# Kernel tuning notes

Measured on AMD Instinct MI355X. Metric: run time of the kernel, lower is better.

The kernel has to match this reference:

```python
import jax, jax.numpy as jnp
import numpy as np

SQ, B, NP, HN = 2048, 2, 16, 64  # [seq, batch, heads, head_dim]

def setup_inputs() -> dict:
    key = jax.random.key(0)
    kq, kk, kv = jax.random.split(key, 3)
    return {
        "query": jax.random.normal(kq, (SQ, B, NP, HN), dtype=jnp.float32),
        "key":   jax.random.normal(kk, (SQ, B, NP, HN), dtype=jnp.float32),
        "value": jax.random.normal(kv, (SQ, B, NP, HN), dtype=jnp.float32),
    }

def reference(query, key, value):
    sq, b, nheads, hn = query.shape
    # NOTE: original module computes norm_factor=sqrt(hn) but never applies it;
    # scores are UNscaled QK^T, replicated faithfully here.
    scores = jnp.einsum('sbnh,tbnh->bnst', query, key)          # [b, np, sq, sk]
    probs = jax.nn.softmax(scores, axis=-1)                      # mask=None -> plain softmax
    # dropout is deterministic (train=False default) -> identity
    context = jnp.einsum('bnst,tbnh->sbnh', probs, value)        # [sq, b, np, hn]
    return context.reshape(sq, b, nheads * hn).astype(jnp.float32)
```

## Files before the change

### kernel.cpp

```cpp
#include <hip/hip_runtime.h>
#include <math.h>
#include <stdint.h>

#define SQ 2048
#define NBH 32
#define HN 64
#define BQ 128
#define BK2 128
#define NP2 (SQ/BK2)
#define TOK 2048
#define HSTRIDE (SQ*HN)

typedef _Float16 half2v __attribute__((ext_vector_type(2)));
typedef _Float16 half4v __attribute__((ext_vector_type(4)));
typedef _Float16 half8v __attribute__((ext_vector_type(8)));
typedef float f32x16 __attribute__((ext_vector_type(16)));

__device__ __forceinline__ void async16(const void* g, void* l) {
  __builtin_amdgcn_global_load_lds(
      (const __attribute__((address_space(1))) void*)g,
      (__attribute__((address_space(3))) void*)l, 16, 0, 0);
}

__device__ __forceinline__ float fexp2(float x) {
#if __has_builtin(__builtin_amdgcn_exp2f)
  return __builtin_amdgcn_exp2f(x);
#else
  return exp2f(x);
#endif
}

__device__ __forceinline__ float xmax32(float x) {
#if __has_builtin(__builtin_amdgcn_permlane32_swap)
  auto r = __builtin_amdgcn_permlane32_swap(__float_as_int(x), __float_as_int(x),
                                            false, false);
  return fmaxf(__int_as_float(r[0]), __int_as_float(r[1]));
#else
  return fmaxf(x, __shfl_xor(x, 32, 64));
#endif
}
__device__ __forceinline__ float xadd32(float x) {
#if __has_builtin(__builtin_amdgcn_permlane32_swap)
  auto r = __builtin_amdgcn_permlane32_swap(__float_as_int(x), __float_as_int(x),
                                            false, false);
  return __int_as_float(r[0]) + __int_as_float(r[1]);
#else
  return x + __shfl_xor(x, 32, 64);
#endif
}

__global__ __launch_bounds__(256) void prep_kv(const float* __restrict__ K,
                                               const float* __restrict__ V,
                                               _Float16* __restrict__ Kh,
                                               _Float16* __restrict__ Vt) {
  __shared__ _Float16 vs[HN * 64];
  const int t = threadIdx.x;
  const int head = blockIdx.y;
  {
    const int key = blockIdx.x * 64 + (t >> 2);
    const int c0 = (t & 3) * 2;
    const float* src = K + (size_t)key * TOK + head * HN + c0 * 8;
    float4 a = *(const float4*)src;
    float4 b = *(const float4*)(src + 4);
    float4 c = *(const float4*)(src + 8);
    float4 d = *(const float4*)(src + 12);
    half8v h0, h1;
    h0[0]=(_Float16)a.x; h0[1]=(_Float16)a.y; h0[2]=(_Float16)a.z; h0[3]=(_Float16)a.w;
    h0[4]=(_Float16)b.x; h0[5]=(_Float16)b.y; h0[6]=(_Float16)b.z; h0[7]=(_Float16)b.w;
    h1[0]=(_Float16)c.x; h1[1]=(_Float16)c.y; h1[2]=(_Float16)c.z; h1[3]=(_Float16)c.w;
    h1[4]=(_Float16)d.x; h1[5]=(_Float16)d.y; h1[6]=(_Float16)d.z; h1[7]=(_Float16)d.w;
    _Float16* row = Kh + (size_t)head * HSTRIDE + (size_t)key * 64;
    *(half8v*)&row[((c0    ) ^ (key & 7)) * 8] = h0;
    *(half8v*)&row[((c0 + 1) ^ (key & 7)) * 8] = h1;
  }
  {
    const int kt = blockIdx.x * 64;
    const int kl = (t >> 3) * 2;
    const int db = (t & 7) * 8;
    const float* src = V + (size_t)(kt + kl) * TOK + head * HN + db;
    float4 a0 = *(const float4*)src;
    float4 a1 = *(const float4*)(src + 4);
    float4 b0 = *(const float4*)(src + TOK);
    float4 b1 = *(const float4*)(src + TOK + 4);
    const float av[8] = {a0.x,a0.y,a0.z,a0.w,a1.x,a1.y,a1.z,a1.w};
    const float bv[8] = {b0.x,b0.y,b0.z,b0.w,b1.x,b1.y,b1.z,b1.w};
    const int u = kl >> 2;
    #pragma unroll
    for (int j = 0; j < 8; ++j) {
      const int dim = db + j;
      const int pos = u ^ (dim & 15);
      half2v h; h[0] = (_Float16)av[j]; h[1] = (_Float16)bv[j];
      *(half2v*)&vs[dim * 64 + pos * 4 + (kl & 3)] = h;
    }
    __syncthreads();
    const int dim = t >> 2;
    const int q = (t & 3) ^ (dim & 3);
    const _Float16* srow = &vs[dim * 64 + q * 16];
    _Float16* drow = Vt + (size_t)head * HSTRIDE + (size_t)dim * SQ + kt + q * 16;
    *(half8v*)&drow[0] = *(const half8v*)&srow[0];
    *(half8v*)&drow[8] = *(const half8v*)&srow[8];
  }
}

__global__ __launch_bounds__(512, 4)
void fattn_mfma(const float* __restrict__ Q, const _Float16* __restrict__ Kh,
                const _Float16* __restrict__ Vt, float* __restrict__ O) {
  __shared__ __align__(16) _Float16 smem[4 * 8192];
  _Float16* kbf = smem;
  _Float16* vtf = smem + 16384;

  const int t = threadIdx.x;
  const int lane = t & 63;
  const int w = t >> 6;
  const int qw = w & 3;
  const int g = w >> 2;
  const int h2 = lane >> 5;
  const int l31 = lane & 31;
  const int q0 = blockIdx.x * BQ + qw * 32;
  const int head = blockIdx.y;
  const _Float16* Kp = Kh + (size_t)head * HSTRIDE;
  const _Float16* Vp = Vt + (size_t)head * HSTRIDE;
  const int tb = g * 4096;

  half8v qf[4];
  {
    const float* qp = Q + (size_t)(q0 + l31) * TOK + head * HN + 8 * h2;
    const float s = 1.44269504088896f;
    #pragma unroll
    for (int ks = 0; ks < 4; ++ks) {
      float4 a = *(const float4*)(qp + 16 * ks);
      float4 b = *(const float4*)(qp + 16 * ks + 4);
      half8v f;
      f[0] = (_Float16)(s*a.x); f[1] = (_Float16)(s*a.y); f[2] = (_Float16)(s*a.z); f[3] = (_Float16)(s*a.w);
      f[4] = (_Float16)(s*b.x); f[5] = (_Float16)(s*b.y); f[6] = (_Float16)(s*b.z); f[7] = (_Float16)(s*b.w);
      qf[ks] = f;
    }
  }

  f32x16 acc0, acc1;
  #pragma unroll
  for (int r = 0; r < 16; ++r) { acc0[r] = 0.f; acc1[r] = 0.f; }
  float m_i = -INFINITY, l_i = 0.f;

  auto stage = [&](int p) {
    const int buf = p & 1;
    const size_t kt = (size_t)p * BK2;
    #pragma unroll
    for (int i = 0; i < 2; ++i) {
      const int off = w * 512 + i * 4096;
      async16(Kp + kt * 64 + off + lane * 8, kbf + buf * 8192 + off);
    }
    #pragma unroll
    for (int tl = 0; tl < 2; ++tl) {
      const int off = w * 512;
      const int eo = off + lane * 8;
      const int dim = eo >> 6, inner = eo & 63;
      async16(Vp + (size_t)dim * SQ + kt + tl * 64 + inner,
              vtf + buf * 8192 + tl * 4096 + off);
    }
  };

  stage(0);
  for (int p = 0; p < NP2; ++p) {
    __syncthreads();
    if (p + 1 < NP2) stage(p + 1);
    const int cur = p & 1;
    const _Float16* kb = kbf + cur * 8192 + tb;
    const _Float16* vb = vtf + cur * 8192 + tb;

    f32x16 c0, c1;
    #pragma unroll
    for (int r = 0; r < 16; ++r) { c0[r] = 0.f; c1[r] = 0.f; }
    #pragma unroll
    for (int ks = 0; ks < 4; ++ks) {
      const int pos = ((h2 + 2 * ks) ^ (l31 & 7)) * 8;
      half8v a0v = *(const half8v*)&kb[l31 * 64 + pos];
      half8v a1v = *(const half8v*)&kb[(l31 + 32) * 64 + pos];
      c0 = __builtin_amdgcn_mfma_f32_32x32x16_f16(a0v, qf[ks], c0, 0, 0, 0);
      c1 = __builtin_amdgcn_mfma_f32_32x32x16_f16(a1v, qf[ks], c1, 0, 0, 0);
    }

    float mx0 = fmaxf(c0[0], c1[0]);
    float mx1 = fmaxf(c0[1], c1[1]);
    float mx2 = fmaxf(c0[2], c1[2]);
    float mx3 = fmaxf(c0[3], c1[3]);
    #pragma unroll
    for (int r = 4; r < 16; r += 4) {
      mx0 = fmaxf(mx0, fmaxf(c0[r],     c1[r]));
      mx1 = fmaxf(mx1, fmaxf(c0[r + 1], c1[r + 1]));
      mx2 = fmaxf(mx2, fmaxf(c0[r + 2], c1[r + 2]));
      mx3 = fmaxf(mx3, fmaxf(c0[r + 3], c1[r + 3]));
    }
    float mx = fmaxf(fmaxf(mx0, mx1), fmaxf(mx2, mx3));
    mx = xmax32(mx);
    const float mnew = fmaxf(m_i, mx);
    const float alpha = fexp2(m_i - mnew);
    float rs0 = 0.f, rs1 = 0.f;
    #pragma unroll
    for (int r = 0; r < 16; ++r) {
      float p0 = fexp2(c0[r] - mnew);
      float p1 = fexp2(c1[r] - mnew);
      c0[r] = p0; c1[r] = p1;
      rs0 += p0; rs1 += p1;
    }
    float rsum = xadd32(rs0 + rs1);
    l_i = l_i * alpha + rsum;
    m_i = mnew;
    #pragma unroll
    for (int r = 0; r < 16; ++r) { acc0[r] *= alpha; acc1[r] *= alpha; }

    #pragma unroll
    for (int ks = 0; ks < 4; ++ks) {
      const int rb = 8 * (ks & 1);
      const f32x16& s = (ks < 2) ? c0 : c1;
      union { half8v v8; half2v v2[4]; } pu;
      #pragma unroll
      for (int tt = 0; tt < 4; ++tt) {
        auto pk = __builtin_amdgcn_cvt_pkrtz(s[rb + 2 * tt], s[rb + 2 * tt + 1]);
        pu.v2[tt] = *(half2v*)&pk;
      }
      #pragma unroll
      for (int mbd = 0; mbd < 2; ++mbd) {
        const int dim = l31 + 32 * mbd;
        const int sw = dim & 15;
        union { half8v v8; half4v v4[2]; } au;
        au.v4[0] = *(const half4v*)&vb[dim * 64 + ((4 * ks + h2)     ^ sw) * 4];
        au.v4[1] = *(const half4v*)&vb[dim * 64 + ((4 * ks + 2 + h2) ^ sw) * 4];
        if (mbd == 0)
          acc0 = __builtin_amdgcn_mfma_f32_32x32x16_f16(au.v8, pu.v8, acc0, 0, 0, 0);
        else
          acc1 = __builtin_amdgcn_mfma_f32_32x32x16_f16(au.v8, pu.v8, acc1, 0, 0, 0);
      }
    }
  }

  __syncthreads();
  float* fb = (float*)smem;
  const int slot = qw * 64 + lane;
  if (g == 1) {
    #pragma unroll
    for (int r = 0; r < 16; ++r) {
      fb[slot * 32 + r]      = acc0[r];
      fb[slot * 32 + 16 + r] = acc1[r];
    }
    fb[8192 + slot] = m_i;
    fb[8448 + slot] = l_i;
  }
  __syncthreads();
  if (g == 0) {
    const float m2 = fb[8192 + slot];
    const float l2 = fb[8448 + slot];
    const float ms = fmaxf(m_i, m2);
    const float a0 = fexp2(m_i - ms);
    const float a1 = fexp2(m2 - ms);
    const float invl = 1.f / (l_i * a0 + l2 * a1);
    float* orow = O + (size_t)(q0 + l31) * TOK + head * HN;
    #pragma unroll
    for (int r = 0; r < 16; ++r) {
      const int d = (r & 3) + 8 * (r >> 2) + 4 * h2;
      orow[d]      = (acc0[r] * a0 + fb[slot * 32 + r]      * a1) * invl;
      orow[d + 32] = (acc1[r] * a0 + fb[slot * 32 + 16 + r] * a1) * invl;
    }
  }
}

extern "C" void kernel_launch(void* const* d_in, const int* in_sizes, int n_in,
                              void* d_out, int out_size, void* d_ws, size_t ws_size,
                              hipStream_t stream) {
  const float* Q = (const float*)d_in[0];
  const float* K = (const float*)d_in[1];
  const float* V = (const float*)d_in[2];
  float* O = (float*)d_out;
  _Float16* Kh = (_Float16*)d_ws;
  _Float16* Vh = Kh + (size_t)NBH * HSTRIDE;
  prep_kv<<<dim3(SQ / 64, NBH), 256, 0, stream>>>(K, V, Kh, Vh);
  fattn_mfma<<<dim3(SQ / BQ, NBH), 512, 0, stream>>>(Q, Kh, Vh, O);
}
```

Measured before the change: 143.0 us.

## Fuse K/V fp16 conversion into attention kernel with register-staged prefetch

Removes the separate prep_kv kernel and its fp16 workspace round trip. The attention kernel now loads fp32 K and V tiles into registers one stage ahead, converts them, and writes them into swizzled/transposed LDS after the softmax step, replacing async global-to-LDS copies. This saves a kernel launch and the extra global traffic. In exchange, each of the 16 query blocks per head rereads fp32 K/V at twice the bytes, register pressure rises (launch bounds drop to 2 blocks), and LDS writes for the V transpose move into the hot loop.

```diff
diff --git a/kernel.cpp b/kernel.cpp
--- a/kernel.cpp
+++ b/kernel.cpp
@@ -9,18 +9,11 @@
 #define BK2 128
 #define NP2 (SQ/BK2)
 #define TOK 2048
-#define HSTRIDE (SQ*HN)
 
 typedef _Float16 half2v __attribute__((ext_vector_type(2)));
 typedef _Float16 half4v __attribute__((ext_vector_type(4)));
 typedef _Float16 half8v __attribute__((ext_vector_type(8)));
 typedef float f32x16 __attribute__((ext_vector_type(16)));
-
-__device__ __forceinline__ void async16(const void* g, void* l) {
-  __builtin_amdgcn_global_load_lds(
-      (const __attribute__((address_space(1))) void*)g,
-      (__attribute__((address_space(3))) void*)l, 16, 0, 0);
-}
 
 __device__ __forceinline__ float fexp2(float x) {
 #if __has_builtin(__builtin_amdgcn_exp2f)
@@ -49,62 +42,9 @@
 #endif
 }
 
-__global__ __launch_bounds__(256) void prep_kv(const float* __restrict__ K,
-                                               const float* __restrict__ V,
-                                               _Float16* __restrict__ Kh,
-                                               _Float16* __restrict__ Vt) {
-  __shared__ _Float16 vs[HN * 64];
-  const int t = threadIdx.x;
-  const int head = blockIdx.y;
-  {
-    const int key = blockIdx.x * 64 + (t >> 2);
-    const int c0 = (t & 3) * 2;
-    const float* src = K + (size_t)key * TOK + head * HN + c0 * 8;
-    float4 a = *(const float4*)src;
-    float4 b = *(const float4*)(src + 4);
-    float4 c = *(const float4*)(src + 8);
-    float4 d = *(const float4*)(src + 12);
-    half8v h0, h1;
-    h0[0]=(_Float16)a.x; h0[1]=(_Float16)a.y; h0[2]=(_Float16)a.z; h0[3]=(_Float16)a.w;
-    h0[4]=(_Float16)b.x; h0[5]=(_Float16)b.y; h0[6]=(_Float16)b.z; h0[7]=(_Float16)b.w;
-    h1[0]=(_Float16)c.x; h1[1]=(_Float16)c.y; h1[2]=(_Float16)c.z; h1[3]=(_Float16)c.w;
-    h1[4]=(_Float16)d.x; h1[5]=(_Float16)d.y; h1[6]=(_Float16)d.z; h1[7]=(_Float16)d.w;
-    _Float16* row = Kh + (size_t)head * HSTRIDE + (size_t)key * 64;
-    *(half8v*)&row[((c0    ) ^ (key & 7)) * 8] = h0;
-    *(half8v*)&row[((c0 + 1) ^ (key & 7)) * 8] = h1;
-  }
-  {
-    const int kt = blockIdx.x * 64;
-    const int kl = (t >> 3) * 2;
-    const int db = (t & 7) * 8;
-    const float* src = V + (size_t)(kt + kl) * TOK + head * HN + db;
-    float4 a0 = *(const float4*)src;
-    float4 a1 = *(const float4*)(src + 4);
-    float4 b0 = *(const float4*)(src + TOK);
-    float4 b1 = *(const float4*)(src + TOK + 4);
-    const float av[8] = {a0.x,a0.y,a0.z,a0.w,a1.x,a1.y,a1.z,a1.w};
-    const float bv[8] = {b0.x,b0.y,b0.z,b0.w,b1.x,b1.y,b1.z,b1.w};
-    const int u = kl >> 2;
-    #pragma unroll
-    for (int j = 0; j < 8; ++j) {
-      const int dim = db + j;
-      const int pos = u ^ (dim & 15);
-      half2v h; h[0] = (_Float16)av[j]; h[1] = (_Float16)bv[j];
-      *(half2v*)&vs[dim * 64 + pos * 4 + (kl & 3)] = h;
-    }
-    __syncthreads();
-    const int dim = t >> 2;
-    const int q = (t & 3) ^ (dim & 3);
-    const _Float16* srow = &vs[dim * 64 + q * 16];
-    _Float16* drow = Vt + (size_t)head * HSTRIDE + (size_t)dim * SQ + kt + q * 16;
-    *(half8v*)&drow[0] = *(const half8v*)&srow[0];
-    *(half8v*)&drow[8] = *(const half8v*)&srow[8];
-  }
-}
-
-__global__ __launch_bounds__(512, 4)
-void fattn_mfma(const float* __restrict__ Q, const _Float16* __restrict__ Kh,
-                const _Float16* __restrict__ Vt, float* __restrict__ O) {
+__global__ __launch_bounds__(512, 2)
+void fattn_fused(const float* __restrict__ Q, const float* __restrict__ K,
+                 const float* __restrict__ V, float* __restrict__ O) {
   __shared__ __align__(16) _Float16 smem[4 * 8192];
   _Float16* kbf = smem;
   _Float16* vtf = smem + 16384;
@@ -118,9 +58,20 @@
   const int l31 = lane & 31;
   const int q0 = blockIdx.x * BQ + qw * 32;
   const int head = blockIdx.y;
-  const _Float16* Kp = Kh + (size_t)head * HSTRIDE;
-  const _Float16* Vp = Vt + (size_t)head * HSTRIDE;
   const int tb = g * 4096;
+
+  const int sk_key = t >> 2;
+  const int sk_c0 = (t & 3) * 2;
+  const int sk_sw0 = ((sk_c0    ) ^ (sk_key & 7)) * 8;
+  const int sk_sw1 = ((sk_c0 + 1) ^ (sk_key & 7)) * 8;
+  const float* ksrc = K + (size_t)sk_key * TOK + head * HN + sk_c0 * 8;
+  const int sv_tl = t >> 8;
+  const int sv_tloc = t & 255;
+  const int sv_kl = (sv_tloc >> 3) * 2;
+  const int sv_db = (sv_tloc & 7) * 8;
+  const int sv_u = sv_kl >> 2;
+  const int sv_k3 = sv_kl & 3;
+  const float* vsrc = V + (size_t)(sv_tl * 64 + sv_kl) * TOK + head * HN + sv_db;
 
   half8v qf[4];
   {
@@ -142,28 +93,52 @@
   for (int r = 0; r < 16; ++r) { acc0[r] = 0.f; acc1[r] = 0.f; }
   float m_i = -INFINITY, l_i = 0.f;
 
-  auto stage = [&](int p) {
+  float4 kr0, kr1, kr2, kr3, vr0, vr1, vr2, vr3;
+
+  auto stage_load = [&](int p) {
+    const size_t off = (size_t)p * BK2 * TOK;
+    const float* ks = ksrc + off;
+    kr0 = *(const float4*)(ks);
+    kr1 = *(const float4*)(ks + 4);
+    kr2 = *(const float4*)(ks + 8);
+    kr3 = *(const float4*)(ks + 12);
+    const float* vs = vsrc + off;
+    vr0 = *(const float4*)(vs);
+    vr1 = *(const float4*)(vs + 4);
+    vr2 = *(const float4*)(vs + TOK);
+    vr3 = *(const float4*)(vs + TOK + 4);
+  };
+  auto stage_write = [&](int p) {
     const int buf = p & 1;
-    const size_t kt = (size_t)p * BK2;
-    #pragma unroll
-    for (int i = 0; i < 2; ++i) {
-      const int off = w * 512 + i * 4096;
-      async16(Kp + kt * 64 + off + lane * 8, kbf + buf * 8192 + off);
-    }
-    #pragma unroll
-    for (int tl = 0; tl < 2; ++tl) {
-      const int off = w * 512;
-      const int eo = off + lane * 8;
-      const int dim = eo >> 6, inner = eo & 63;
-      async16(Vp + (size_t)dim * SQ + kt + tl * 64 + inner,
-              vtf + buf * 8192 + tl * 4096 + off);
+    {
+      half8v h0, h1;
+      h0[0]=(_Float16)kr0.x; h0[1]=(_Float16)kr0.y; h0[2]=(_Float16)kr0.z; h0[3]=(_Float16)kr0.w;
+      h0[4]=(_Float16)kr1.x; h0[5]=(_Float16)kr1.y; h0[6]=(_Float16)kr1.z; h0[7]=(_Float16)kr1.w;
+      h1[0]=(_Float16)kr2.x; h1[1]=(_Float16)kr2.y; h1[2]=(_Float16)kr2.z; h1[3]=(_Float16)kr2.w;
+      h1[4]=(_Float16)kr3.x; h1[5]=(_Float16)kr3.y; h1[6]=(_Float16)kr3.z; h1[7]=(_Float16)kr3.w;
+      _Float16* row = kbf + buf * 8192 + sk_key * 64;
+      *(half8v*)&row[sk_sw0] = h0;
+      *(half8v*)&row[sk_sw1] = h1;
+    }
+    {
+      const float av[8] = {vr0.x,vr0.y,vr0.z,vr0.w,vr1.x,vr1.y,vr1.z,vr1.w};
+      const float bv[8] = {vr2.x,vr2.y,vr2.z,vr2.w,vr3.x,vr3.y,vr3.z,vr3.w};
+      _Float16* vrow = vtf + buf * 8192 + sv_tl * 4096;
+      #pragma unroll
+      for (int j = 0; j < 8; ++j) {
+        const int dim = sv_db + j;
+        const int pos = sv_u ^ (dim & 15);
+        half2v h; h[0] = (_Float16)av[j]; h[1] = (_Float16)bv[j];
+        *(half2v*)&vrow[dim * 64 + pos * 4 + sv_k3] = h;
+      }
     }
   };
 
-  stage(0);
+  stage_load(0);
+  stage_write(0);
   for (int p = 0; p < NP2; ++p) {
     __syncthreads();
-    if (p + 1 < NP2) stage(p + 1);
+    if (p + 1 < NP2) stage_load(p + 1);
     const int cur = p & 1;
     const _Float16* kb = kbf + cur * 8192 + tb;
     const _Float16* vb = vtf + cur * 8192 + tb;
@@ -208,6 +183,8 @@
     m_i = mnew;
     #pragma unroll
     for (int r = 0; r < 16; ++r) { acc0[r] *= alpha; acc1[r] *= alpha; }
+
+    if (p + 1 < NP2) stage_write(p + 1);
 
     #pragma unroll
     for (int ks = 0; ks < 4; ++ks) {
@@ -271,8 +248,6 @@
   const float* K = (const float*)d_in[1];
   const float* V = (const float*)d_in[2];
   float* O = (float*)d_out;
-  _Float16* Kh = (_Float16*)d_ws;
-  _Float16* Vh = Kh + (size_t)NBH * HSTRIDE;
-  prep_kv<<<dim3(SQ / 64, NBH), 256, 0, stream>>>(K, V, Kh, Vh);
-  fattn_mfma<<<dim3(SQ / BQ, NBH), 512, 0, stream>>>(Q, Kh, Vh, O);
-}
+  (void)d_ws; (void)ws_size;
+  fattn_fused<<<dim3(SQ / BQ, NBH), 512, 0, stream>>>(Q, K, V, O);
+}
```

After: 167.3 us. +17.0%, slower.

## Process two 32-row query tiles per wave to reuse K/V LDS fragments

Applied to the files above, without the earlier changes.

Each wave now handles 64 query rows (two 32-row sub-tiles A and B) instead of 32, doubling the block query tile to 256. Each K and V fragment read from LDS feeds two MFMAs, halving LDS traffic and K/V global staging per query row. The cost is doubled accumulator and score register pressure, so launch bounds drop to 2 blocks per CU. The grid also halves to 256 blocks, which may under-fill the GPU, and the epilogue merge becomes serialized with extra barriers.

```diff
diff --git a/kernel.cpp b/kernel.cpp
--- a/kernel.cpp
+++ b/kernel.cpp
@@ -5,7 +5,7 @@
 #define SQ 2048
 #define NBH 32
 #define HN 64
-#define BQ 128
+#define BQ 256
 #define BK2 128
 #define NP2 (SQ/BK2)
 #define TOK 2048
@@ -102,7 +102,7 @@
   }
 }
 
-__global__ __launch_bounds__(512, 4)
+__global__ __launch_bounds__(512, 2)
 void fattn_mfma(const float* __restrict__ Q, const _Float16* __restrict__ Kh,
                 const _Float16* __restrict__ Vt, float* __restrict__ O) {
   __shared__ __align__(16) _Float16 smem[4 * 8192];
@@ -116,31 +116,37 @@
   const int g = w >> 2;
   const int h2 = lane >> 5;
   const int l31 = lane & 31;
-  const int q0 = blockIdx.x * BQ + qw * 32;
+  const int q0 = blockIdx.x * BQ + qw * 64;
   const int head = blockIdx.y;
   const _Float16* Kp = Kh + (size_t)head * HSTRIDE;
   const _Float16* Vp = Vt + (size_t)head * HSTRIDE;
   const int tb = g * 4096;
 
-  half8v qf[4];
+  half8v qfA[4], qfB[4];
   {
-    const float* qp = Q + (size_t)(q0 + l31) * TOK + head * HN + 8 * h2;
     const float s = 1.44269504088896f;
+    const float* qpA = Q + (size_t)(q0 + l31) * TOK + head * HN + 8 * h2;
+    const float* qpB = qpA + (size_t)32 * TOK;
     #pragma unroll
     for (int ks = 0; ks < 4; ++ks) {
-      float4 a = *(const float4*)(qp + 16 * ks);
-      float4 b = *(const float4*)(qp + 16 * ks + 4);
+      float4 a = *(const float4*)(qpA + 16 * ks);
+      float4 b = *(const float4*)(qpA + 16 * ks + 4);
       half8v f;
       f[0] = (_Float16)(s*a.x); f[1] = (_Float16)(s*a.y); f[2] = (_Float16)(s*a.z); f[3] = (_Float16)(s*a.w);
       f[4] = (_Float16)(s*b.x); f[5] = (_Float16)(s*b.y); f[6] = (_Float16)(s*b.z); f[7] = (_Float16)(s*b.w);
-      qf[ks] = f;
-    }
-  }
-
-  f32x16 acc0, acc1;
+      qfA[ks] = f;
+      a = *(const float4*)(qpB + 16 * ks);
+      b = *(const float4*)(qpB + 16 * ks + 4);
+      f[0] = (_Float16)(s*a.x); f[1] = (_Float16)(s*a.y); f[2] = (_Float16)(s*a.z); f[3] = (_Float16)(s*a.w);
+      f[4] = (_Float16)(s*b.x); f[5] = (_Float16)(s*b.y); f[6] = (_Float16)(s*b.z); f[7] = (_Float16)(s*b.w);
+      qfB[ks] = f;
+    }
+  }
+
+  f32x16 accA0, accA1, accB0, accB1;
   #pragma unroll
-  for (int r = 0; r < 16; ++r) { acc0[r] = 0.f; acc1[r] = 0.f; }
-  float m_i = -INFINITY, l_i = 0.f;
+  for (int r = 0; r < 16; ++r) { accA0[r]=0.f; accA1[r]=0.f; accB0[r]=0.f; accB1[r]=0.f; }
+  float mA = -INFINITY, lA = 0.f, mB = -INFINITY, lB = 0.f;
 
   auto stage = [&](int p) {
     const int buf = p & 1;
@@ -168,56 +174,89 @@
     const _Float16* kb = kbf + cur * 8192 + tb;
     const _Float16* vb = vtf + cur * 8192 + tb;
 
-    f32x16 c0, c1;
-    #pragma unroll
-    for (int r = 0; r < 16; ++r) { c0[r] = 0.f; c1[r] = 0.f; }
+    f32x16 cA0, cA1, cB0, cB1;
+    #pragma unroll
+    for (int r = 0; r < 16; ++r) { cA0[r]=0.f; cA1[r]=0.f; cB0[r]=0.f; cB1[r]=0.f; }
     #pragma unroll
     for (int ks = 0; ks < 4; ++ks) {
       const int pos = ((h2 + 2 * ks) ^ (l31 & 7)) * 8;
       half8v a0v = *(const half8v*)&kb[l31 * 64 + pos];
       half8v a1v = *(const half8v*)&kb[(l31 + 32) * 64 + pos];
-      c0 = __builtin_amdgcn_mfma_f32_32x32x16_f16(a0v, qf[ks], c0, 0, 0, 0);
-      c1 = __builtin_amdgcn_mfma_f32_32x32x16_f16(a1v, qf[ks], c1, 0, 0, 0);
-    }
-
-    float mx0 = fmaxf(c0[0], c1[0]);
-    float mx1 = fmaxf(c0[1], c1[1]);
-    float mx2 = fmaxf(c0[2], c1[2]);
-    float mx3 = fmaxf(c0[3], c1[3]);
-    #pragma unroll
-    for (int r = 4; r < 16; r += 4) {
-      mx0 = fmaxf(mx0, fmaxf(c0[r],     c1[r]));
-      mx1 = fmaxf(mx1, fmaxf(c0[r + 1], c1[r + 1]));
-      mx2 = fmaxf(mx2, fmaxf(c0[r + 2], c1[r + 2]));
-      mx3 = fmaxf(mx3, fmaxf(c0[r + 3], c1[r + 3]));
-    }
-    float mx = fmaxf(fmaxf(mx0, mx1), fmaxf(mx2, mx3));
-    mx = xmax32(mx);
-    const float mnew = fmaxf(m_i, mx);
-    const float alpha = fexp2(m_i - mnew);
-    float rs0 = 0.f, rs1 = 0.f;
-    #pragma unroll
-    for (int r = 0; r < 16; ++r) {
-      float p0 = fexp2(c0[r] - mnew);
-      float p1 = fexp2(c1[r] - mnew);
-      c0[r] = p0; c1[r] = p1;
-      rs0 += p0; rs1 += p1;
-    }
-    float rsum = xadd32(rs0 + rs1);
-    l_i = l_i * alpha + rsum;
-    m_i = mnew;
-    #pragma unroll
-    for (int r = 0; r < 16; ++r) { acc0[r] *= alpha; acc1[r] *= alpha; }
+      cA0 = __builtin_amdgcn_mfma_f32_32x32x16_f16(a0v, qfA[ks], cA0, 0, 0, 0);
+      cB0 = __builtin_amdgcn_mfma_f32_32x32x16_f16(a0v, qfB[ks], cB0, 0, 0, 0);
+      cA1 = __builtin_amdgcn_mfma_f32_32x32x16_f16(a1v, qfA[ks], cA1, 0, 0, 0);
+      cB1 = __builtin_amdgcn_mfma_f32_32x32x16_f16(a1v, qfB[ks], cB1, 0, 0, 0);
+    }
+
+    {
+      float mx0 = fmaxf(cA0[0], cA1[0]);
+      float mx1 = fmaxf(cA0[1], cA1[1]);
+      float mx2 = fmaxf(cA0[2], cA1[2]);
+      float mx3 = fmaxf(cA0[3], cA1[3]);
+      #pragma unroll
+      for (int r = 4; r < 16; r += 4) {
+        mx0 = fmaxf(mx0, fmaxf(cA0[r],     cA1[r]));
+        mx1 = fmaxf(mx1, fmaxf(cA0[r + 1], cA1[r + 1]));
+        mx2 = fmaxf(mx2, fmaxf(cA0[r + 2], cA1[r + 2]));
+        mx3 = fmaxf(mx3, fmaxf(cA0[r + 3], cA1[r + 3]));
+      }
+      float mx = xmax32(fmaxf(fmaxf(mx0, mx1), fmaxf(mx2, mx3)));
+      const float mnew = fmaxf(mA, mx);
+      const float alpha = fexp2(mA - mnew);
+      float rs0 = 0.f, rs1 = 0.f;
+      #pragma unroll
+      for (int r = 0; r < 16; ++r) {
+        float p0 = fexp2(cA0[r] - mnew);
+        float p1 = fexp2(cA1[r] - mnew);
+        cA0[r] = p0; cA1[r] = p1;
+        rs0 += p0; rs1 += p1;
+      }
+      lA = lA * alpha + xadd32(rs0 + rs1);
+      mA = mnew;
+      #pragma unroll
+      for (int r = 0; r < 16; ++r) { accA0[r] *= alpha; accA1[r] *= alpha; }
+    }
+    {
+      float mx0 = fmaxf(cB0[0], cB1[0]);
+      float mx1 = fmaxf(cB0[1], cB1[1]);
+      float mx2 = fmaxf(cB0[2], cB1[2]);
+      float mx3 = fmaxf(cB0[3], cB1[3]);
+      #pragma unroll
+      for (int r = 4; r < 16; r += 4) {
+        mx0 = fmaxf(mx0, fmaxf(cB0[r],     cB1[r]));
+        mx1 = fmaxf(mx1, fmaxf(cB0[r + 1], cB1[r + 1]));
+        mx2 = fmaxf(mx2, fmaxf(cB0[r + 2], cB1[r + 2]));
+        mx3 = fmaxf(mx3, fmaxf(cB0[r + 3], cB1[r + 3]));
+      }
+      float mx = xmax32(fmaxf(fmaxf(mx0, mx1), fmaxf(mx2, mx3)));
+      const float mnew = fmaxf(mB, mx);
+      const float alpha = fexp2(mB - mnew);
+      float rs0 = 0.f, rs1 = 0.f;
+      #pragma unroll
+      for (int r = 0; r < 16; ++r) {
+        float p0 = fexp2(cB0[r] - mnew);
+        float p1 = fexp2(cB1[r] - mnew);
+        cB0[r] = p0; cB1[r] = p1;
+        rs0 += p0; rs1 += p1;
+      }
+      lB = lB * alpha + xadd32(rs0 + rs1);
+      mB = mnew;
+      #pragma unroll
+      for (int r = 0; r < 16; ++r) { accB0[r] *= alpha; accB1[r] *= alpha; }
+    }
 
     #pragma unroll
     for (int ks = 0; ks < 4; ++ks) {
       const int rb = 8 * (ks & 1);
-      const f32x16& s = (ks < 2) ? c0 : c1;
-      union { half8v v8; half2v v2[4]; } pu;
+      const f32x16& sA = (ks < 2) ? cA0 : cA1;
+      const f32x16& sB = (ks < 2) ? cB0 : cB1;
+      union { half8v v8; half2v v2[4]; } puA, puB;
       #pragma unroll
       for (int tt = 0; tt < 4; ++tt) {
-        auto pk = __builtin_amdgcn_cvt_pkrtz(s[rb + 2 * tt], s[rb + 2 * tt + 1]);
-        pu.v2[tt] = *(half2v*)&pk;
+        auto pkA = __builtin_amdgcn_cvt_pkrtz(sA[rb + 2 * tt], sA[rb + 2 * tt + 1]);
+        puA.v2[tt] = *(half2v*)&pkA;
+        auto pkB = __builtin_amdgcn_cvt_pkrtz(sB[rb + 2 * tt], sB[rb + 2 * tt + 1]);
+        puB.v2[tt] = *(half2v*)&pkB;
       }
       #pragma unroll
       for (int mbd = 0; mbd < 2; ++mbd) {
@@ -226,40 +265,69 @@
         union { half8v v8; half4v v4[2]; } au;
         au.v4[0] = *(const half4v*)&vb[dim * 64 + ((4 * ks + h2)     ^ sw) * 4];
         au.v4[1] = *(const half4v*)&vb[dim * 64 + ((4 * ks + 2 + h2) ^ sw) * 4];
-        if (mbd == 0)
-          acc0 = __builtin_amdgcn_mfma_f32_32x32x16_f16(au.v8, pu.v8, acc0, 0, 0, 0);
-        else
-          acc1 = __builtin_amdgcn_mfma_f32_32x32x16_f16(au.v8, pu.v8, acc1, 0, 0, 0);
-      }
-    }
-  }
-
-  __syncthreads();
+        if (mbd == 0) {
+          accA0 = __builtin_amdgcn_mfma_f32_32x32x16_f16(au.v8, puA.v8, accA0, 0, 0, 0);
+          accB0 = __builtin_amdgcn_mfma_f32_32x32x16_f16(au.v8, puB.v8, accB0, 0, 0, 0);
+        } else {
+          accA1 = __builtin_amdgcn_mfma_f32_32x32x16_f16(au.v8, puA.v8, accA1, 0, 0, 0);
+          accB1 = __builtin_amdgcn_mfma_f32_32x32x16_f16(au.v8, puB.v8, accB1, 0, 0, 0);
+        }
+      }
+    }
+  }
+
   float* fb = (float*)smem;
   const int slot = qw * 64 + lane;
+  __syncthreads();
   if (g == 1) {
     #pragma unroll
     for (int r = 0; r < 16; ++r) {
-      fb[slot * 32 + r]      = acc0[r];
-      fb[slot * 32 + 16 + r] = acc1[r];
-    }
-    fb[8192 + slot] = m_i;
-    fb[8448 + slot] = l_i;
+      fb[slot * 32 + r]      = accA0[r];
+      fb[slot * 32 + 16 + r] = accA1[r];
+    }
+    fb[8192 + slot] = mA;
+    fb[8448 + slot] = lA;
   }
   __syncthreads();
   if (g == 0) {
     const float m2 = fb[8192 + slot];
     const float l2 = fb[8448 + slot];
-    const float ms = fmaxf(m_i, m2);
-    const float a0 = fexp2(m_i - ms);
+    const float ms = fmaxf(mA, m2);
+    const float a0 = fexp2(mA - ms);
     const float a1 = fexp2(m2 - ms);
-    const float invl = 1.f / (l_i * a0 + l2 * a1);
+    const float invl = 1.f / (lA * a0 + l2 * a1);
     float* orow = O + (size_t)(q0 + l31) * TOK + head * HN;
     #pragma unroll
     for (int r = 0; r < 16; ++r) {
       const int d = (r & 3) + 8 * (r >> 2) + 4 * h2;
-      orow[d]      = (acc0[r] * a0 + fb[slot * 32 + r]      * a1) * invl;
-      orow[d + 32] = (acc1[r] * a0 + fb[slot * 32 + 16 + r] * a1) * invl;
+      orow[d]      = (accA0[r] * a0 + fb[slot * 32 + r]      * a1) * invl;
+      orow[d + 32] = (accA1[r] * a0 + fb[slot * 32 + 16 + r] * a1) * invl;
+    }
+  }
+  __syncthreads();
+  if (g == 1) {
+    #pragma unroll
+    for (int r = 0; r < 16; ++r) {
+      fb[slot * 32 + r]      = accB0[r];
+      fb[slot * 32 + 16 + r] = accB1[r];
+    }
+    fb[8192 + slot] = mB;
+    fb[8448 + slot] = lB;
+  }
+  __syncthreads();
+  if (g == 0) {
+    const float m2 = fb[8192 + slot];
+    const float l2 = fb[8448 + slot];
+    const float ms = fmaxf(mB, m2);
+    const float a0 = fexp2(mB - ms);
+    const float a1 = fexp2(m2 - ms);
+    const float invl = 1.f / (lB * a0 + l2 * a1);
+    float* orow = O + (size_t)(q0 + 32 + l31) * TOK + head * HN;
+    #pragma unroll
+    for (int r = 0; r < 16; ++r) {
+      const int d = (r & 3) + 8 * (r >> 2) + 4 * h2;
+      orow[d]      = (accB0[r] * a0 + fb[slot * 32 + r]      * a1) * invl;
+      orow[d + 32] = (accB1[r] * a0 + fb[slot * 32 + 16 + r] * a1) * invl;
     }
   }
 }
```

New measurement: 143.6 us. Within noise of the previous version (+0.5%).

## Double key tile per stage and interleave two QK/softmax/PV subtiles per warp

Applied to the files above, without the earlier changes.

Each pipeline stage now loads 256 keys instead of 128, so every warp group handles two 64-key subtiles per iteration. Both QK MFMAs are issued before the softmax/PV phases, which gives more independent MFMA work to overlap with the exp and reduction math. The loop also runs half as many iterations, so there are fewer barriers. In exchange, shared memory grows to 128KB (now dynamic), launch bounds drop to 2 blocks per SM, and more accumulators stay live, which lowers occupancy.

```diff
diff --git a/kernel.cpp b/kernel.cpp
--- a/kernel.cpp
+++ b/kernel.cpp
@@ -6,8 +6,8 @@
 #define NBH 32
 #define HN 64
 #define BQ 128
-#define BK2 128
-#define NP2 (SQ/BK2)
+#define BK4 256
+#define NP4 (SQ/BK4)
 #define TOK 2048
 #define HSTRIDE (SQ*HN)
 
@@ -102,12 +102,12 @@
   }
 }
 
-__global__ __launch_bounds__(512, 4)
+__global__ __launch_bounds__(512, 2)
 void fattn_mfma(const float* __restrict__ Q, const _Float16* __restrict__ Kh,
                 const _Float16* __restrict__ Vt, float* __restrict__ O) {
-  __shared__ __align__(16) _Float16 smem[4 * 8192];
+  extern __shared__ __align__(16) _Float16 smem[];
   _Float16* kbf = smem;
-  _Float16* vtf = smem + 16384;
+  _Float16* vtf = smem + 32768;
 
   const int t = threadIdx.x;
   const int lane = t & 63;
@@ -120,7 +120,6 @@
   const int head = blockIdx.y;
   const _Float16* Kp = Kh + (size_t)head * HSTRIDE;
   const _Float16* Vp = Vt + (size_t)head * HSTRIDE;
-  const int tb = g * 4096;
 
   half8v qf[4];
   {
@@ -144,31 +143,23 @@
 
   auto stage = [&](int p) {
     const int buf = p & 1;
-    const size_t kt = (size_t)p * BK2;
-    #pragma unroll
-    for (int i = 0; i < 2; ++i) {
+    const size_t kt = (size_t)p * BK4;
+    #pragma unroll
+    for (int i = 0; i < 4; ++i) {
       const int off = w * 512 + i * 4096;
-      async16(Kp + kt * 64 + off + lane * 8, kbf + buf * 8192 + off);
-    }
-    #pragma unroll
-    for (int tl = 0; tl < 2; ++tl) {
+      async16(Kp + kt * 64 + off + lane * 8, kbf + buf * 16384 + off);
+    }
+    #pragma unroll
+    for (int tl = 0; tl < 4; ++tl) {
       const int off = w * 512;
       const int eo = off + lane * 8;
       const int dim = eo >> 6, inner = eo & 63;
       async16(Vp + (size_t)dim * SQ + kt + tl * 64 + inner,
-              vtf + buf * 8192 + tl * 4096 + off);
-    }
-  };
-
-  stage(0);
-  for (int p = 0; p < NP2; ++p) {
-    __syncthreads();
-    if (p + 1 < NP2) stage(p + 1);
-    const int cur = p & 1;
-    const _Float16* kb = kbf + cur * 8192 + tb;
-    const _Float16* vb = vtf + cur * 8192 + tb;
-
-    f32x16 c0, c1;
+              vtf + buf * 16384 + tl * 4096 + off);
+    }
+  };
+
+  auto qk_tile = [&](const _Float16* kb, f32x16& c0, f32x16& c1) {
     #pragma unroll
     for (int r = 0; r < 16; ++r) { c0[r] = 0.f; c1[r] = 0.f; }
     #pragma unroll
@@ -179,7 +170,9 @@
       c0 = __builtin_amdgcn_mfma_f32_32x32x16_f16(a0v, qf[ks], c0, 0, 0, 0);
       c1 = __builtin_amdgcn_mfma_f32_32x32x16_f16(a1v, qf[ks], c1, 0, 0, 0);
     }
-
+  };
+
+  auto smax = [&](f32x16& c0, f32x16& c1) {
     float mx0 = fmaxf(c0[0], c1[0]);
     float mx1 = fmaxf(c0[1], c1[1]);
     float mx2 = fmaxf(c0[2], c1[2]);
@@ -191,8 +184,7 @@
       mx2 = fmaxf(mx2, fmaxf(c0[r + 2], c1[r + 2]));
       mx3 = fmaxf(mx3, fmaxf(c0[r + 3], c1[r + 3]));
     }
-    float mx = fmaxf(fmaxf(mx0, mx1), fmaxf(mx2, mx3));
-    mx = xmax32(mx);
+    float mx = xmax32(fmaxf(fmaxf(mx0, mx1), fmaxf(mx2, mx3)));
     const float mnew = fmaxf(m_i, mx);
     const float alpha = fexp2(m_i - mnew);
     float rs0 = 0.f, rs1 = 0.f;
@@ -203,12 +195,13 @@
       c0[r] = p0; c1[r] = p1;
       rs0 += p0; rs1 += p1;
     }
-    float rsum = xadd32(rs0 + rs1);
-    l_i = l_i * alpha + rsum;
+    l_i = l_i * alpha + xadd32(rs0 + rs1);
     m_i = mnew;
     #pragma unroll
     for (int r = 0; r < 16; ++r) { acc0[r] *= alpha; acc1[r] *= alpha; }
-
+  };
+
+  auto pv_tile = [&](const _Float16* vb, const f32x16& c0, const f32x16& c1) {
     #pragma unroll
     for (int ks = 0; ks < 4; ++ks) {
       const int rb = 8 * (ks & 1);
@@ -232,6 +225,25 @@
           acc1 = __builtin_amdgcn_mfma_f32_32x32x16_f16(au.v8, pu.v8, acc1, 0, 0, 0);
       }
     }
+  };
+
+  stage(0);
+  for (int p = 0; p < NP4; ++p) {
+    __syncthreads();
+    if (p + 1 < NP4) stage(p + 1);
+    const int cur = p & 1;
+    const _Float16* kb0 = kbf + cur * 16384 + (2 * g    ) * 4096;
+    const _Float16* kb1 = kbf + cur * 16384 + (2 * g + 1) * 4096;
+    const _Float16* vb0 = vtf + cur * 16384 + (2 * g    ) * 4096;
+    const _Float16* vb1 = vtf + cur * 16384 + (2 * g + 1) * 4096;
+
+    f32x16 s0, s1, u0, u1;
+    qk_tile(kb0, s0, s1);
+    qk_tile(kb1, u0, u1);
+    smax(s0, s1);
+    pv_tile(vb0, s0, s1);
+    smax(u0, u1);
+    pv_tile(vb1, u0, u1);
   }
 
   __syncthreads();
@@ -273,6 +285,12 @@
   float* O = (float*)d_out;
   _Float16* Kh = (_Float16*)d_ws;
   _Float16* Vh = Kh + (size_t)NBH * HSTRIDE;
+  static bool attr_done = false;
+  if (!attr_done) {
+    hipFuncSetAttribute(reinterpret_cast<const void*>(fattn_mfma),
+                        hipFuncAttributeMaxDynamicSharedMemorySize, 131072);
+    attr_done = true;
+  }
   prep_kv<<<dim3(SQ / 64, NBH), 256, 0, stream>>>(K, V, Kh, Vh);
-  fattn_mfma<<<dim3(SQ / BQ, NBH), 512, 0, stream>>>(Q, Kh, Vh, O);
-}
+  fattn_mfma<<<dim3(SQ / BQ, NBH), 512, 131072, stream>>>(Q, Kh, Vh, O);
+}
```

Measured after the change: 149.6 us. 4.6% more time.
